# Kernel optimization log

Hardware: AMD Instinct MI355X
Metric: run time of the kernel (lower is better)

The kernel has to match this reference:

```python
import jax, jax.numpy as jnp
import numpy as np

S, IN, M, V, K = 8192, 512, 512, 50, 8


def setup_inputs() -> dict:
    key = jax.random.key(0)
    ks = jax.random.split(key, 6)
    sc = 0.02
    inp = {
        "inputs": jax.random.normal(ks[0], (S, IN), jnp.float32),
        "Wioux": sc * jax.random.normal(ks[1], (5 * M, IN), jnp.float32),
        "bioux": jnp.zeros((5 * M,), jnp.float32),
        "Wiouh": sc * jax.random.normal(ks[2], (5 * M, M), jnp.float32),
        "biouh": jnp.zeros((5 * M,), jnp.float32),
        "Wlx": sc * jax.random.normal(ks[3], (M, IN), jnp.float32),
        "blx": jnp.zeros((M,), jnp.float32),
        "Wlh": sc * jax.random.normal(ks[4], (M, M), jnp.float32),
        "blh": jnp.zeros((M,), jnp.float32),
        "lb": jnp.ones((V, M), jnp.float32),  # nn.Parameter(torch.ones(V, M))
    }
    rng = np.random.default_rng(0)
    t = np.arange(S)[:, None]
    u1 = rng.random((S, K)); u2 = rng.random((S, K))
    rel_fw = (u1 * np.maximum(t, 1)).astype(np.int32)                     # idx < t
    rel_bw = np.minimum(t + 1 + (u2 * np.maximum(S - 1 - t, 1)).astype(np.int64), S - 1).astype(np.int32)  # idx > t
    mask_fw = rng.random((S, K)) < 0.6
    mask_fw[0, :] = False      # t=0 fwd has no relatives in the original
    mask_bw = rng.random((S, K)) < 0.6
    mask_bw[S - 1, :] = False  # t=S-1 bwd has no relatives
    inp["rel_fw"] = jnp.asarray(rel_fw)
    inp["dep_fw"] = jnp.asarray(rng.integers(0, V, (S, K)).astype(np.int32))
    inp["mask_fw"] = jnp.asarray(mask_fw)
    inp["rel_bw"] = jnp.asarray(rel_bw)
    inp["dep_bw"] = jnp.asarray(rng.integers(0, V, (S, K)).astype(np.int32))
    inp["mask_bw"] = jnp.asarray(mask_bw)
    return inp


def _syn_lstm(inputs, Wioux, bioux, Wiouh, biouh, Wlx, blx, Wlh, blh, lb,
              rel, dep, mask, order):
    """One direction; order gives the timestep visit order. Returns [S, M]."""
    mdim = Wlh.shape[0]

    def step(carry, t):
        Hbuf, h_prev, c_prev = carry
        x = inputs[t]
        ious = Wioux @ x + bioux + Wiouh @ h_prev + biouh          # [5M]
        c0, c1, c2, c3, c4 = jnp.split(ious, 5)
        # NOTE: original torch code assigns (i,o,f,s,u)=(sig(i),sig(o),sig(s),sig(f),tanh(u)),
        # i.e. gate f uses chunk 3 and gate s uses chunk 2 -- reproduced faithfully.
        i = jax.nn.sigmoid(c0)
        o = jax.nn.sigmoid(c1)
        f = jax.nn.sigmoid(c3)
        s = jax.nn.sigmoid(c2)
        u = jnp.tanh(c4)
        c = f * c_prev + i * u
        h = o * jnp.tanh(c)
        rel_h = Hbuf[rel[t]]                                       # [K, M] gather of prior hiddens
        l = jax.nn.sigmoid(rel_h @ Wlh.T + blh + (Wlx @ x + blx) + lb[dep[t]])  # [K, M]
        agg = jnp.sum(l * rel_h * mask[t][:, None].astype(rel_h.dtype), axis=0)  # [M]
        h = h + s * jnp.tanh(agg)   # if all masked: agg=0, tanh(0)=0 -> empty-relative branch
        Hbuf = Hbuf.at[t].set(h)
        return (Hbuf, h, c), None

    Hbuf0 = jnp.zeros((inputs.shape[0], mdim), inputs.dtype)
    z = jnp.zeros((mdim,), inputs.dtype)
    (Hbuf, _, _), _ = jax.lax.scan(step, (Hbuf0, z, z), order)
    return Hbuf


def reference(inputs, Wioux, bioux, Wiouh, biouh, Wlx, blx, Wlh, blh, lb,
              rel_fw, dep_fw, mask_fw, rel_bw, dep_bw, mask_bw):
    n = inputs.shape[0]
    Hfw = _syn_lstm(inputs, Wioux, bioux, Wiouh, biouh, Wlx, blx, Wlh, blh, lb,
                    rel_fw, dep_fw, mask_fw, jnp.arange(n))
    Hbw = _syn_lstm(inputs, Wioux, bioux, Wiouh, biouh, Wlx, blx, Wlh, blh, lb,
                    rel_bw, dep_bw, mask_bw, jnp.arange(n - 1, -1, -1))
    return jnp.concatenate([Hfw, Hbw], axis=1)   # [S, 2*M]
```

## Files before the change

### kernel.cpp

```cpp
#include <hip/hip_runtime.h>

#define S_LEN 8192
#define KREL 8
#define WPD 64

typedef float f4 __attribute__((ext_vector_type(4)));
typedef unsigned long long u64;

__device__ __forceinline__ float sigmf(float x) { return 1.0f / (1.0f + __expf(-x)); }
__device__ __forceinline__ float tanhfast(float x) { return 1.0f - 2.0f / (__expf(2.0f * x) + 1.0f); }

__global__ void k_maskcvt(const unsigned char* __restrict__ src,
                          unsigned char* __restrict__ dst, int n)
{
  const unsigned int* w = (const unsigned int*)src;
  __shared__ int s_i32, s_f32;
  if (threadIdx.x == 0) { s_i32 = 1; s_f32 = 1; }
  __syncthreads();
  int i32ok = 1, f32ok = 1;
  for (int i = threadIdx.x; i < 1024; i += blockDim.x) {
    const unsigned int v = w[i];
    if (v != 0u && v != 1u) i32ok = 0;
    if (v != 0u && v != 0x3F800000u) f32ok = 0;
  }
  if (!i32ok) atomicAnd(&s_i32, 0);
  if (!f32ok) atomicAnd(&s_f32, 0);
  __syncthreads();
  const int wide = (s_i32 || s_f32);
  for (int i = blockIdx.x * blockDim.x + threadIdx.x; i < n; i += gridDim.x * blockDim.x)
    dst[i] = wide ? (w[i] ? 1 : 0) : (src[i] ? 1 : 0);
}

__global__ __launch_bounds__(256)
void k_gemm(const float* __restrict__ X, const float* __restrict__ Wioux,
            const float* __restrict__ Wlx, const float* __restrict__ bioux,
            const float* __restrict__ biouh, const float* __restrict__ blx,
            const float* __restrict__ blh, float* __restrict__ P)
{
  __shared__ float As[16][64];
  __shared__ float Bs[16][64];
  const int t0 = blockIdx.x * 64;
  const int r0 = blockIdx.y * 64;
  const int tid = threadIdx.x;
  const int tx = tid & 15, ty = tid >> 4;
  const int si = tid >> 2, sk = (tid & 3) << 2;
  const int rB = r0 + si;
  const float* brow = (rB < 2560) ? (Wioux + (size_t)rB * 512)
                                  : (Wlx + (size_t)(rB - 2560) * 512);
  const float* arow = X + (size_t)(t0 + si) * 512;
  float acc[4][4] = {};
  for (int k0 = 0; k0 < 512; k0 += 16) {
    const float4 av = *(const float4*)(arow + k0 + sk);
    const float4 bv = *(const float4*)(brow + k0 + sk);
    __syncthreads();
    As[sk + 0][si] = av.x; As[sk + 1][si] = av.y; As[sk + 2][si] = av.z; As[sk + 3][si] = av.w;
    Bs[sk + 0][si] = bv.x; Bs[sk + 1][si] = bv.y; Bs[sk + 2][si] = bv.z; Bs[sk + 3][si] = bv.w;
    __syncthreads();
#pragma unroll
    for (int kk = 0; kk < 16; ++kk) {
      const float4 a = *(const float4*)&As[kk][ty * 4];
      const float4 b = *(const float4*)&Bs[kk][tx * 4];
      acc[0][0] += a.x * b.x; acc[0][1] += a.x * b.y; acc[0][2] += a.x * b.z; acc[0][3] += a.x * b.w;
      acc[1][0] += a.y * b.x; acc[1][1] += a.y * b.y; acc[1][2] += a.y * b.z; acc[1][3] += a.y * b.w;
      acc[2][0] += a.z * b.x; acc[2][1] += a.z * b.y; acc[2][2] += a.z * b.z; acc[2][3] += a.z * b.w;
      acc[3][0] += a.w * b.x; acc[3][1] += a.w * b.y; acc[3][2] += a.w * b.z; acc[3][3] += a.w * b.w;
    }
  }
#pragma unroll
  for (int i = 0; i < 4; ++i) {
    const int t = t0 + ty * 4 + i;
#pragma unroll
    for (int j = 0; j < 4; ++j) {
      const int r = r0 + tx * 4 + j;
      const float bias = (r < 2560) ? (bioux[r] + biouh[r]) : (blx[r - 2560] + blh[r - 2560]);
      P[(size_t)t * 3072 + r] = acc[i][j] + bias;
    }
  }
}

__global__ __launch_bounds__(512, 1)
void k_rec(const float* __restrict__ Wiouh, const float* __restrict__ Wlh,
           const float* __restrict__ P, const float* __restrict__ lb,
           const int* __restrict__ rel_fw, const int* __restrict__ dep_fw,
           const unsigned char* __restrict__ mask_fw,
           const int* __restrict__ rel_bw, const int* __restrict__ dep_bw,
           const unsigned char* __restrict__ mask_bw,
           float* __restrict__ Gfw, float* __restrict__ Gbw,
           u64* rec, float* __restrict__ out)
{
  __shared__ u64 hsp[2][2][4][64];
  const int wg  = blockIdx.x;
  const int dir = wg / WPD;
  const int w   = wg % WPD;
  const int tid = threadIdx.x;
  const int grp = tid >> 6;
  const int lane = tid & 63;
  const int kl = lane & 7;
  const int m = w * 8 + grp;
  const int dircol = dir * 512;
  const int* rel = dir ? rel_bw : rel_fw;
  const int* dep = dir ? dep_bw : dep_fw;
  const unsigned char* msk = dir ? mask_bw : mask_fw;
  float* Gbuf = dir ? Gbw : Gfw;

  f4 wreg[6][2];
  {
    const float* rows[6];
#pragma unroll
    for (int rg = 0; rg < 5; ++rg) rows[rg] = Wiouh + (size_t)(rg * 512 + m) * 512;
    rows[5] = Wlh + (size_t)m * 512;
#pragma unroll
    for (int rg = 0; rg < 6; ++rg)
#pragma unroll
      for (int q = 0; q < 2; ++q)
        wreg[rg][q] = *(const f4*)(rows[rg] + q * 256 + lane * 4);
  }

  {
    u64* hz = (u64*)hsp;
    hz[tid] = 0ull; hz[tid + 512] = 0ull;
  }

  float cstate = 0.0f, hprev = 0.0f, gprev = 0.0f;

  int jjU, mkU, jjN, mkN, depN;
  float Hg, Gg, LBg;
  float p0, p1, p2, p3, p4, p5;
  {
    const int t0 = dir ? (S_LEN - 1) : 0;
    const int t1 = dir ? (S_LEN - 2) : 1;
    jjU = rel[t0 * KREL + kl]; mkU = (int)msk[t0 * KREL + kl];
    Hg  = out[(size_t)jjU * 1024 + dircol + m];
    Gg  = Gbuf[(size_t)jjU * 512 + m];
    LBg = lb[(size_t)dep[t0 * KREL + kl] * 512 + m];
    const float* prow = P + (size_t)t0 * 3072;
    p0 = prow[m];        p1 = prow[512 + m];  p2 = prow[1024 + m];
    p3 = prow[1536 + m]; p4 = prow[2048 + m]; p5 = prow[2560 + m];
    jjN = rel[t1 * KREL + kl]; mkN = (int)msk[t1 * KREL + kl]; depN = dep[t1 * KREL + kl];
  }
  __syncthreads();

#pragma unroll 1
  for (int s = 0; s < S_LEN; ++s) {
    const int t = dir ? (S_LEN - 1 - s) : s;
    const int tn = dir ? (t - 1) : (t + 1);
    const int prevt  = dir ? (t + 1) : (t - 1);
    const int prevt2 = dir ? (t + 2) : (t - 2);
    const int par = s & 1;

    if (s > 0) {
      const int pb = (((s - 1) & 1) * 2 + dir) * 512;
      u64* q0 = rec + pb + tid;
      u64 a0 = __hip_atomic_load(q0, __ATOMIC_RELAXED, __HIP_MEMORY_SCOPE_AGENT);
      u64 b0 = __hip_atomic_load(q0, __ATOMIC_RELAXED, __HIP_MEMORY_SCOPE_AGENT);
      u64 c0 = __hip_atomic_load(q0, __ATOMIC_RELAXED, __HIP_MEMORY_SCOPE_AGENT);
      for (;;) {
        if ((unsigned)(a0 >> 32) >= (unsigned)s) break;
        __builtin_amdgcn_s_sleep(2);
        const u64 n0 = __hip_atomic_load(q0, __ATOMIC_RELAXED, __HIP_MEMORY_SCOPE_AGENT);
        a0 = b0;  b0 = c0;  c0 = n0;
      }
      const int half = tid >> 8;
      const int idx  = tid & 255;
      __hip_atomic_store(&hsp[par][half][idx & 3][idx >> 2], a0,
                         __ATOMIC_RELAXED, __HIP_MEMORY_SCOPE_WORKGROUP);
    }

    u64 pk0[4], pk1[4];
    for (;;) {
      unsigned mn = 0xffffffffu;
#pragma unroll
      for (int j = 0; j < 4; ++j) {
        pk0[j] = __hip_atomic_load(&hsp[par][0][j][lane],
                                   __ATOMIC_RELAXED, __HIP_MEMORY_SCOPE_WORKGROUP);
        pk1[j] = __hip_atomic_load(&hsp[par][1][j][lane],
                                   __ATOMIC_RELAXED, __HIP_MEMORY_SCOPE_WORKGROUP);
        const unsigned t0 = (unsigned)(pk0[j] >> 32);
        const unsigned t1 = (unsigned)(pk1[j] >> 32);
        mn = mn < t0 ? mn : t0;
        mn = mn < t1 ? mn : t1;
      }
      if (mn >= (unsigned)s) break;
    }

    float hx0[4], hx1[4];
#pragma unroll
    for (int j = 0; j < 4; ++j) {
      hx0[j] = __uint_as_float((unsigned)pk0[j]);
      hx1[j] = __uint_as_float((unsigned)pk1[j]);
    }
    float dsum[6];
#pragma unroll
    for (int rg = 0; rg < 6; ++rg) {
      float a = 0.0f;
#pragma unroll
      for (int j = 0; j < 4; ++j) {
        a += wreg[rg][0][j] * hx0[j];
        a += wreg[rg][1][j] * hx1[j];
      }
      a += __shfl_xor(a, 1);  a += __shfl_xor(a, 2);  a += __shfl_xor(a, 4);
      a += __shfl_xor(a, 8);  a += __shfl_xor(a, 16); a += __shfl_xor(a, 32);
      dsum[rg] = a;
    }
    const float g = dsum[5];

    const float iv = sigmf(p0 + dsum[0]);
    const float ov = sigmf(p1 + dsum[1]);
    const float sv = sigmf(p2 + dsum[2]);
    const float fv = sigmf(p3 + dsum[3]);
    const float uv = tanhfast(p4 + dsum[4]);
    cstate = fv * cstate + iv * uv;
    const float hb = ov * tanhfast(cstate);

    const float hv_k = (jjU == prevt) ? hprev : Hg;
    const float gv_k = (jjU == prevt) ? g : ((jjU == prevt2) ? gprev : Gg);
    float sm = mkU ? (sigmf(gv_k + p5 + LBg) * hv_k) : 0.0f;
    sm += __shfl_xor(sm, 1); sm += __shfl_xor(sm, 2); sm += __shfl_xor(sm, 4);
    const float hval = hb + sv * tanhfast(sm);

    if (lane == 0) {
      const u64 pk =
          ((u64)(unsigned)(s + 1) << 32) | (u64)__float_as_uint(hval);
      __hip_atomic_store(rec + ((s & 1) * 2 + dir) * 512 + m, pk,
                         __ATOMIC_RELAXED, __HIP_MEMORY_SCOPE_AGENT);
      out[(size_t)t * 1024 + dircol + m] = hval;
      if (s > 0) Gbuf[(size_t)prevt * 512 + m] = g;
    }

    if (s < S_LEN - 1) {
      const float HgN  = out[(size_t)jjN * 1024 + dircol + m];
      const float GgN  = Gbuf[(size_t)jjN * 512 + m];
      const float LBgN = lb[(size_t)depN * 512 + m];
      const float* prow = P + (size_t)tn * 3072;
      p0 = prow[m];        p1 = prow[512 + m];  p2 = prow[1024 + m];
      p3 = prow[1536 + m]; p4 = prow[2048 + m]; p5 = prow[2560 + m];
      int jj2 = jjN, mk2 = mkN, dep2 = depN;
      if (s < S_LEN - 2) {
        const int t2 = dir ? (t - 2) : (t + 2);
        jj2 = rel[t2 * KREL + kl]; mk2 = (int)msk[t2 * KREL + kl]; dep2 = dep[t2 * KREL + kl];
      }
      jjU = jjN; mkU = mkN; Hg = HgN; Gg = GgN; LBg = LBgN;
      jjN = jj2; mkN = mk2; depN = dep2;
    }
    hprev = hval; gprev = g;
  }
}

__global__ void k_fill(float* __restrict__ o, int n, float v)
{ const int i = blockIdx.x * 256 + threadIdx.x; if (i < n) o[i] = v; }

extern "C" void kernel_launch(void* const* d_in, const int* in_sizes, int n_in,
                              void* d_out, int out_size, void* d_ws, size_t ws_size,
                              hipStream_t stream)
{
  (void)in_sizes; (void)n_in;
  const float* X     = (const float*)d_in[0];
  const float* Wioux = (const float*)d_in[1];
  const float* bioux = (const float*)d_in[2];
  const float* Wiouh = (const float*)d_in[3];
  const float* biouh = (const float*)d_in[4];
  const float* Wlx   = (const float*)d_in[5];
  const float* blx   = (const float*)d_in[6];
  const float* Wlh   = (const float*)d_in[7];
  const float* blh   = (const float*)d_in[8];
  const float* lb    = (const float*)d_in[9];
  const int* rel_fw  = (const int*)d_in[10];
  const int* dep_fw  = (const int*)d_in[11];
  const unsigned char* mask_fw_raw = (const unsigned char*)d_in[12];
  const int* rel_bw  = (const int*)d_in[13];
  const int* dep_bw  = (const int*)d_in[14];
  const unsigned char* mask_bw_raw = (const unsigned char*)d_in[15];
  float* out = (float*)d_out;

  const int nmask = S_LEN * KREL;
  const size_t needP = (size_t)S_LEN * 3072 * 4;
  const size_t needG = (size_t)S_LEN * 512 * 4;
  const size_t need  = 32768 + needP + 2 * needG + 2 * (size_t)nmask;
  if (ws_size < need) {
    k_fill<<<(out_size + 255) / 256, 256, 0, stream>>>(out, out_size, 12345.0f);
    return;
  }
  char* ws = (char*)d_ws;
  u64*   rec = (u64*)ws;
  float* P   = (float*)(ws + 32768);
  float* Gfw = (float*)(ws + 32768 + needP);
  float* Gbw = Gfw + (size_t)S_LEN * 512;
  unsigned char* Mfw = (unsigned char*)(ws + 32768 + needP + 2 * needG);
  unsigned char* Mbw = Mfw + nmask;

  hipMemsetAsync(rec, 0, 16384, stream);
  k_maskcvt<<<64, 256, 0, stream>>>(mask_fw_raw, Mfw, nmask);
  k_maskcvt<<<64, 256, 0, stream>>>(mask_bw_raw, Mbw, nmask);
  dim3 gg(S_LEN / 64, 3072 / 64);
  k_gemm<<<gg, 256, 0, stream>>>(X, Wioux, Wlx, bioux, biouh, blx, blh, P);
  k_rec<<<2 * WPD, 512, 0, stream>>>(Wiouh, Wlh, P, lb, rel_fw, dep_fw, Mfw,
                                     rel_bw, dep_bw, Mbw, Gfw, Gbw, rec, out);
}
```

Measured before the change: 20.00 ms.

## Poll global hidden state directly per wave, drop shared-memory relay

The recurrent kernel now runs 256 workgroups of 256 threads, four hidden units each, instead of 128 workgroups of 512 threads. Each wave polls all 512 published hidden values straight from the global rec buffer, using eight loads per lane and a min-check on the step tags. This removes the shared-memory relay and the intra-workgroup LDS spin. Producers write to a permuted publish index so each lane receives the elements it needs, at the cost of eight times more global polling traffic per wave and twice as many workgroups that must be co-resident for the spin-wait scheme to work.

```diff
diff --git a/kernel.cpp b/kernel.cpp
--- a/kernel.cpp
+++ b/kernel.cpp
@@ -2,7 +2,7 @@
 
 #define S_LEN 8192
 #define KREL 8
-#define WPD 64
+#define WPD 128
 
 typedef float f4 __attribute__((ext_vector_type(4)));
 typedef unsigned long long u64;
@@ -78,7 +78,7 @@
   }
 }
 
-__global__ __launch_bounds__(512, 1)
+__global__ __launch_bounds__(256, 1)
 void k_rec(const float* __restrict__ Wiouh, const float* __restrict__ Wlh,
            const float* __restrict__ P, const float* __restrict__ lb,
            const int* __restrict__ rel_fw, const int* __restrict__ dep_fw,
@@ -88,7 +88,6 @@
            float* __restrict__ Gfw, float* __restrict__ Gbw,
            u64* rec, float* __restrict__ out)
 {
-  __shared__ u64 hsp[2][2][4][64];
   const int wg  = blockIdx.x;
   const int dir = wg / WPD;
   const int w   = wg % WPD;
@@ -96,13 +95,15 @@
   const int grp = tid >> 6;
   const int lane = tid & 63;
   const int kl = lane & 7;
-  const int m = w * 8 + grp;
+  const int m = w * 4 + grp;
   const int dircol = dir * 512;
   const int* rel = dir ? rel_bw : rel_fw;
   const int* dep = dir ? dep_bw : dep_fw;
   const unsigned char* msk = dir ? mask_bw : mask_fw;
   float* Gbuf = dir ? Gbw : Gfw;
 
+  const int pub_idx = ((m >> 8) << 8) + ((m & 3) << 6) + ((m & 255) >> 2);
+
   f4 wreg[6][2];
   {
     const float* rows[6];
@@ -114,11 +115,6 @@
 #pragma unroll
       for (int q = 0; q < 2; ++q)
         wreg[rg][q] = *(const f4*)(rows[rg] + q * 256 + lane * 4);
-  }
-
-  {
-    u64* hz = (u64*)hsp;
-    hz[tid] = 0ull; hz[tid + 512] = 0ull;
   }
 
   float cstate = 0.0f, hprev = 0.0f, gprev = 0.0f;
@@ -138,7 +134,6 @@
     p3 = prow[1536 + m]; p4 = prow[2048 + m]; p5 = prow[2560 + m];
     jjN = rel[t1 * KREL + kl]; mkN = (int)msk[t1 * KREL + kl]; depN = dep[t1 * KREL + kl];
   }
-  __syncthreads();
 
 #pragma unroll 1
   for (int s = 0; s < S_LEN; ++s) {
@@ -146,48 +141,42 @@
     const int tn = dir ? (t - 1) : (t + 1);
     const int prevt  = dir ? (t + 1) : (t - 1);
     const int prevt2 = dir ? (t + 2) : (t - 2);
-    const int par = s & 1;
-
-    if (s > 0) {
+
+    u64 g0[8], g1[8], g2[8];
+    {
       const int pb = (((s - 1) & 1) * 2 + dir) * 512;
-      u64* q0 = rec + pb + tid;
-      u64 a0 = __hip_atomic_load(q0, __ATOMIC_RELAXED, __HIP_MEMORY_SCOPE_AGENT);
-      u64 b0 = __hip_atomic_load(q0, __ATOMIC_RELAXED, __HIP_MEMORY_SCOPE_AGENT);
-      u64 c0 = __hip_atomic_load(q0, __ATOMIC_RELAXED, __HIP_MEMORY_SCOPE_AGENT);
+      u64* base = rec + pb + lane;
+#pragma unroll
+      for (int k = 0; k < 8; ++k)
+        g0[k] = __hip_atomic_load(base + k * 64, __ATOMIC_RELAXED, __HIP_MEMORY_SCOPE_AGENT);
+#pragma unroll
+      for (int k = 0; k < 8; ++k)
+        g1[k] = __hip_atomic_load(base + k * 64, __ATOMIC_RELAXED, __HIP_MEMORY_SCOPE_AGENT);
+#pragma unroll
+      for (int k = 0; k < 8; ++k)
+        g2[k] = __hip_atomic_load(base + k * 64, __ATOMIC_RELAXED, __HIP_MEMORY_SCOPE_AGENT);
       for (;;) {
-        if ((unsigned)(a0 >> 32) >= (unsigned)s) break;
+        unsigned mn = 0xffffffffu;
+#pragma unroll
+        for (int k = 0; k < 8; ++k) {
+          const unsigned tg = (unsigned)(g0[k] >> 32);
+          mn = mn < tg ? mn : tg;
+        }
+        if (mn >= (unsigned)s) break;
         __builtin_amdgcn_s_sleep(2);
-        const u64 n0 = __hip_atomic_load(q0, __ATOMIC_RELAXED, __HIP_MEMORY_SCOPE_AGENT);
-        a0 = b0;  b0 = c0;  c0 = n0;
+#pragma unroll
+        for (int k = 0; k < 8; ++k) {
+          g0[k] = g1[k]; g1[k] = g2[k];
+          g2[k] = __hip_atomic_load(base + k * 64, __ATOMIC_RELAXED, __HIP_MEMORY_SCOPE_AGENT);
+        }
       }
-      const int half = tid >> 8;
-      const int idx  = tid & 255;
-      __hip_atomic_store(&hsp[par][half][idx & 3][idx >> 2], a0,
-                         __ATOMIC_RELAXED, __HIP_MEMORY_SCOPE_WORKGROUP);
-    }
-
-    u64 pk0[4], pk1[4];
-    for (;;) {
-      unsigned mn = 0xffffffffu;
-#pragma unroll
-      for (int j = 0; j < 4; ++j) {
-        pk0[j] = __hip_atomic_load(&hsp[par][0][j][lane],
-                                   __ATOMIC_RELAXED, __HIP_MEMORY_SCOPE_WORKGROUP);
-        pk1[j] = __hip_atomic_load(&hsp[par][1][j][lane],
-                                   __ATOMIC_RELAXED, __HIP_MEMORY_SCOPE_WORKGROUP);
-        const unsigned t0 = (unsigned)(pk0[j] >> 32);
-        const unsigned t1 = (unsigned)(pk1[j] >> 32);
-        mn = mn < t0 ? mn : t0;
-        mn = mn < t1 ? mn : t1;
-      }
-      if (mn >= (unsigned)s) break;
     }
 
     float hx0[4], hx1[4];
 #pragma unroll
     for (int j = 0; j < 4; ++j) {
-      hx0[j] = __uint_as_float((unsigned)pk0[j]);
-      hx1[j] = __uint_as_float((unsigned)pk1[j]);
+      hx0[j] = __uint_as_float((unsigned)g0[j]);
+      hx1[j] = __uint_as_float((unsigned)g0[4 + j]);
     }
     float dsum[6];
 #pragma unroll
@@ -221,7 +210,7 @@
     if (lane == 0) {
       const u64 pk =
           ((u64)(unsigned)(s + 1) << 32) | (u64)__float_as_uint(hval);
-      __hip_atomic_store(rec + ((s & 1) * 2 + dir) * 512 + m, pk,
+      __hip_atomic_store(rec + ((s & 1) * 2 + dir) * 512 + pub_idx, pk,
                          __ATOMIC_RELAXED, __HIP_MEMORY_SCOPE_AGENT);
       out[(size_t)t * 1024 + dircol + m] = hval;
       if (s > 0) Gbuf[(size_t)prevt * 512 + m] = g;
@@ -293,6 +282,6 @@
   k_maskcvt<<<64, 256, 0, stream>>>(mask_bw_raw, Mbw, nmask);
   dim3 gg(S_LEN / 64, 3072 / 64);
   k_gemm<<<gg, 256, 0, stream>>>(X, Wioux, Wlx, bioux, biouh, blx, blh, P);
-  k_rec<<<2 * WPD, 512, 0, stream>>>(Wiouh, Wlh, P, lb, rel_fw, dep_fw, Mfw,
+  k_rec<<<2 * WPD, 256, 0, stream>>>(Wiouh, Wlh, P, lb, rel_fw, dep_fw, Mfw,
                                      rel_bw, dep_bw, Mbw, Gfw, Gbw, rec, out);
 }
```

Measured after the change: 36.31 ms. +81.6%, slower.
